# Kernel optimization log

Measured on AMD Instinct MI355X. Metric: run time of the kernel, lower is better.

## Reference

```python
import jax, jax.numpy as jnp
import numpy as np

B, C, M = 1024, 64, 512  # batch, cluster_dim, num_clusters


def setup_inputs() -> dict:
    key = jax.random.key(0)
    k1, k2, k3 = jax.random.split(key, 3)
    x = jax.random.normal(k1, (B, C, M), dtype=jnp.float32)
    running_mean = jax.random.normal(k2, (1, C, M), dtype=jnp.float32) * 0.1
    # per-cluster whitening subspaces: identity + small symmetric perturbation
    A = jax.random.normal(k3, (M, C, C), dtype=jnp.float32) * 0.05
    subspaces = jnp.eye(C, dtype=jnp.float32)[None] + 0.5 * (A + jnp.swapaxes(A, -1, -2))
    return {"x": x, "running_mean": running_mean, "subspaces": subspaces}


def reference(x, running_mean, subspaces):
    # ZCANormSVDPI inference forward:
    #   x: (B, C, M); running_mean: (1, C, M); subspaces: (M, C, C)
    #   xc = x - running_mean; per-cluster m: z[m] = subspaces[m] @ xc[:, :, m]^T
    #   output permuted back to (B, C, M)
    xc = x - running_mean                      # (B, C, M)
    z = jnp.einsum('mcd,bdm->bcm', subspaces, xc)  # (B, C, M)
    return z
```

## Files before the change

kernel.cpp:

```cpp
#include <hip/hip_runtime.h>


typedef __attribute__((ext_vector_type(8))) short short8;
typedef __attribute__((ext_vector_type(4))) float f32x4;

namespace {
constexpr int Mm = 512, Cc = 64, Bb = 1024;
constexpr int MT = 16;
constexpr int BT = 16;
constexpr int NB = 8;
constexpr int ZR = 20;
constexpr size_t LDSB = 2 * 32768 + 1024 * ZR * 4;

__device__ __forceinline__ unsigned short f2bf(float v) {
  unsigned uu = __float_as_uint(v);
  uu = (uu + 0x7fffu + ((uu >> 16) & 1u)) >> 16;
  return (unsigned short)uu;
}
__device__ __forceinline__ unsigned pack2(float a, float b) {
  return (unsigned)f2bf(a) | ((unsigned)f2bf(b) << 16);
}
__device__ __forceinline__ int xsw(int row, int chunk) {
  return chunk ^ (row & 7) ^ (((row >> 6) & 3) << 1);
}
}

#define ELEM(V, I) \
  ((I) == 0 ? (V).x : (I) == 1 ? (V).y : (I) == 2 ? (V).z : (V).w)

__global__ __launch_bounds__(1024, 4) void zca_pipe(
    const float* __restrict__ x, const float* __restrict__ mean,
    const float* __restrict__ S, float* __restrict__ out) {
  extern __shared__ unsigned char lds[];
  unsigned char* xbuf0 = lds;
  unsigned char* xbuf1 = lds + 32768;
  float* zl = (float*)(lds + 65536);

  const int tid = threadIdx.x;
  const int l = tid & 63;
  const int w = __builtin_amdgcn_readfirstlane(tid >> 6);

  const int id = blockIdx.x;
  const int sw = ((id & 7) << 5) + (id >> 3);
  const int m0 = (sw >> 3) * MT;
  const int bg = (sw & 7) * (BT * NB);

  const int mq = tid & 3;
  const int u = (tid >> 2) & 15;
  const int d2 = ((w & 1) << 5) + (u << 1);
  const int bq = w >> 1;
  const int chunkS = ((w & 1) << 2) + (u >> 2);
  const int rowB = (w << 4) + (l & 15);
  const int rs = tid >> 2;

  float4 st0[4], st1[4];

#define ISSUE(ST, T)                                                          \
  {                                                                           \
    _Pragma("unroll") for (int dd = 0; dd < 2; ++dd)                          \
        _Pragma("unroll") for (int p = 0; p < 2; ++p)                         \
            ST[dd * 2 + p] = *(const float4*)(                                \
                x + (size_t)((bg + (T)*BT + p * 8 + bq) * Cc + d2 + dd) * Mm  \
                  + m0 + mq * 4);                                             \
  }

#define STAGE(ST, XW)                                                         \
  {                                                                           \
    _Pragma("unroll") for (int p = 0; p < 2; ++p) {                           \
      _Pragma("unroll") for (int i = 0; i < 4; ++i) {                         \
        const int row = (mq * 4 + i) * BT + p * 8 + bq;                       \
        const unsigned v = pack2(ELEM(ST[p], i) - ELEM(mv0, i),               \
                                 ELEM(ST[2 + p], i) - ELEM(mv1, i));          \
        *(unsigned*)((XW) + row * 128 + xsw(row, chunkS) * 16 + (u & 3) * 4) = \
            v;                                                                \
      }                                                                       \
    }                                                                         \
  }

#define BAR()                                           \
  {                                                     \
    asm volatile("s_waitcnt lgkmcnt(0)" ::: "memory");  \
    __builtin_amdgcn_s_barrier();                       \
  }

#define ZW(CT, R, AC)                                                   \
  {                                                                     \
    const int c_ = (CT)*16 + (l >> 4) * 4 + (R);                        \
    const int zrow = c_ * 16 + (l & 15);                                \
    const int col = (((w >> 2) ^ ((zrow >> 6) & 3)) << 2) + (w & 3);    \
    zl[zrow * ZR + col] = (AC)[(R)];                                    \
  }

  ISSUE(st0, 0)
  ISSUE(st1, 1)
  const float4 mv0 = *(const float4*)(mean + (size_t)d2 * Mm + m0 + mq * 4);
  const float4 mv1 =
      *(const float4*)(mean + (size_t)(d2 + 1) * Mm + m0 + mq * 4);

  short8 A[4][2];
#pragma unroll
  for (int ct = 0; ct < 4; ++ct) {
#pragma unroll
    for (int ks = 0; ks < 2; ++ks) {
      const float* sp = S + ((size_t)(m0 + w) * Cc + ct * 16 + (l & 15)) * Cc +
                        ks * 32 + (l >> 4) * 8;
      const float4 f0 = *(const float4*)sp;
      const float4 f1 = *(const float4*)(sp + 4);
      short8 a;
      a[0] = (short)f2bf(f0.x); a[1] = (short)f2bf(f0.y);
      a[2] = (short)f2bf(f0.z); a[3] = (short)f2bf(f0.w);
      a[4] = (short)f2bf(f1.x); a[5] = (short)f2bf(f1.y);
      a[6] = (short)f2bf(f1.z); a[7] = (short)f2bf(f1.w);
      A[ct][ks] = a;
    }
  }
  STAGE(st0, xbuf0)
  BAR()

#define ITER(T, STC, STN)                                                      \
  {                                                                            \
    const unsigned char* xr = ((T)&1) ? xbuf1 : xbuf0;                         \
    unsigned char* xw = ((T)&1) ? xbuf0 : xbuf1;                               \
    const short8 Bf0 =                                                         \
        *(const short8*)(xr + rowB * 128 + xsw(rowB, (l >> 4)) * 16);          \
    const short8 Bf1 =                                                         \
        *(const short8*)(xr + rowB * 128 + xsw(rowB, 4 + (l >> 4)) * 16);      \
    if ((T) + 2 < NB) ISSUE(STN, (T) + 2)                                      \
    f32x4 ac0 = {0.f, 0.f, 0.f, 0.f}, ac1 = {0.f, 0.f, 0.f, 0.f},              \
          ac2 = {0.f, 0.f, 0.f, 0.f}, ac3 = {0.f, 0.f, 0.f, 0.f};              \
    ac0 = __builtin_amdgcn_mfma_f32_16x16x32_bf16(A[0][0], Bf0, ac0, 0, 0, 0); \
    ac1 = __builtin_amdgcn_mfma_f32_16x16x32_bf16(A[1][0], Bf0, ac1, 0, 0, 0); \
    ac2 = __builtin_amdgcn_mfma_f32_16x16x32_bf16(A[2][0], Bf0, ac2, 0, 0, 0); \
    ac3 = __builtin_amdgcn_mfma_f32_16x16x32_bf16(A[3][0], Bf0, ac3, 0, 0, 0); \
    ac0 = __builtin_amdgcn_mfma_f32_16x16x32_bf16(A[0][1], Bf1, ac0, 0, 0, 0); \
    ac1 = __builtin_amdgcn_mfma_f32_16x16x32_bf16(A[1][1], Bf1, ac1, 0, 0, 0); \
    ac2 = __builtin_amdgcn_mfma_f32_16x16x32_bf16(A[2][1], Bf1, ac2, 0, 0, 0); \
    ac3 = __builtin_amdgcn_mfma_f32_16x16x32_bf16(A[3][1], Bf1, ac3, 0, 0, 0); \
    if ((T) + 1 < NB) STAGE(STC, xw)                                           \
    BAR()                                                                      \
    _Pragma("unroll") for (int r = 0; r < 4; ++r) {                            \
      ZW(0, r, ac0) ZW(1, r, ac1) ZW(2, r, ac2) ZW(3, r, ac3)                  \
    }                                                                          \
    BAR()                                                                      \
    _Pragma("unroll") for (int t2 = 0; t2 < 4; ++t2) {                         \
      const int row = t2 * 256 + rs;                                           \
      const int qd = mq ^ ((row >> 6) & 3);                                    \
      const float4 v = *(const float4*)(zl + row * ZR + qd * 4);               \
      *(float4*)(out + (size_t)((bg + (T)*BT + (row & 15)) * Cc +              \
                                (row >> 4)) * Mm + m0 + mq * 4) = v;           \
    }                                                                          \
  }

  ITER(0, st1, st0)
  ITER(1, st0, st1)
  ITER(2, st1, st0)
  ITER(3, st0, st1)
  ITER(4, st1, st0)
  ITER(5, st0, st1)
  ITER(6, st1, st0)
  ITER(7, st0, st1)

#undef ITER
#undef ZW
#undef BAR
#undef STAGE
#undef ISSUE
}

extern "C" void kernel_launch(void* const* d_in, const int* in_sizes, int n_in,
                              void* d_out, int out_size, void* d_ws,
                              size_t ws_size, hipStream_t stream) {
  const float* x = (const float*)d_in[0];
  const float* mean = (const float*)d_in[1];
  const float* S = (const float*)d_in[2];
  float* out = (float*)d_out;
  const int nblocks = (Mm / MT) * (Bb / (BT * NB));
  hipLaunchKernelGGL(zca_pipe, dim3(nblocks), dim3(1024), LDSB, stream, x,
                     mean, S, out);
}
```

Baseline: 74.93 us.

## Halve cluster tile to 8 with 512-thread blocks and single LDS buffer

```diff
diff --git a/kernel.cpp b/kernel.cpp
--- a/kernel.cpp
+++ b/kernel.cpp
@@ -6,11 +6,11 @@
 
 namespace {
 constexpr int Mm = 512, Cc = 64, Bb = 1024;
-constexpr int MT = 16;
+constexpr int MT = 8;
 constexpr int BT = 16;
 constexpr int NB = 8;
-constexpr int ZR = 20;
-constexpr size_t LDSB = 2 * 32768 + 1024 * ZR * 4;
+constexpr int ZP = 12;
+constexpr size_t LDSB = 128 * 128 + 1024 * ZP * 4;
 
 __device__ __forceinline__ unsigned short f2bf(float v) {
   unsigned uu = __float_as_uint(v);
@@ -20,82 +20,67 @@
 __device__ __forceinline__ unsigned pack2(float a, float b) {
   return (unsigned)f2bf(a) | ((unsigned)f2bf(b) << 16);
 }
-__device__ __forceinline__ int xsw(int row, int chunk) {
-  return chunk ^ (row & 7) ^ (((row >> 6) & 3) << 1);
-}
 }
 
 #define ELEM(V, I) \
   ((I) == 0 ? (V).x : (I) == 1 ? (V).y : (I) == 2 ? (V).z : (V).w)
 
-__global__ __launch_bounds__(1024, 4) void zca_pipe(
+__global__ __launch_bounds__(512, 4) void zca_v7(
     const float* __restrict__ x, const float* __restrict__ mean,
     const float* __restrict__ S, float* __restrict__ out) {
   extern __shared__ unsigned char lds[];
-  unsigned char* xbuf0 = lds;
-  unsigned char* xbuf1 = lds + 32768;
-  float* zl = (float*)(lds + 65536);
+  unsigned char* xl = lds;
+  float* zl = (float*)(lds + 16384);
 
   const int tid = threadIdx.x;
   const int l = tid & 63;
   const int w = __builtin_amdgcn_readfirstlane(tid >> 6);
 
   const int id = blockIdx.x;
-  const int sw = ((id & 7) << 5) + (id >> 3);
+  const int sw = ((id & 7) << 6) + (id >> 3);
   const int m0 = (sw >> 3) * MT;
-  const int bg = (sw & 7) * (BT * NB);
+  const int b0 = (sw & 7) * (BT * NB);
 
-  const int mq = tid & 3;
-  const int u = (tid >> 2) & 15;
-  const int d2 = ((w & 1) << 5) + (u << 1);
-  const int bq = w >> 1;
-  const int chunkS = ((w & 1) << 2) + (u >> 2);
-  const int rowB = (w << 4) + (l & 15);
-  const int rs = tid >> 2;
+  const int mq = l & 1;
+  const int e = l >> 1;
+  const int g2 = w >> 1;
+
+#define ISSUE(ST, T)                                                         \
+  {                                                                          \
+    _Pragma("unroll") for (int dd = 0; dd < 2; ++dd)                         \
+        _Pragma("unroll") for (int p = 0; p < 2; ++p)                        \
+            ST[dd * 2 + p] = *(const float4*)(                               \
+                x + (size_t)((b0 + (T)*BT + p * 8 + w) * Cc + 2 * e + dd) *  \
+                        Mm + m0 + mq * 4);                                   \
+  }
+
+#define STAGE(ST)                                                            \
+  {                                                                          \
+    _Pragma("unroll") for (int p = 0; p < 2; ++p) {                          \
+      _Pragma("unroll") for (int i = 0; i < 4; ++i) {                        \
+        const int row = (mq * 4 + i) * BT + p * 8 + w;                       \
+        const unsigned v = pack2(ELEM(ST[p], i) - ELEM(mvE, i),              \
+                                 ELEM(ST[2 + p], i) - ELEM(mvO, i));         \
+        *(unsigned*)(xl + row * 128 + (((e >> 2) ^ w) << 4) +                \
+                     ((e & 3) << 2)) = v;                                    \
+      }                                                                      \
+    }                                                                        \
+  }
+
+#define BAR()                                          \
+  {                                                    \
+    asm volatile("s_waitcnt lgkmcnt(0)" ::: "memory"); \
+    __builtin_amdgcn_s_barrier();                      \
+  }
 
   float4 st0[4], st1[4];
 
-#define ISSUE(ST, T)                                                          \
-  {                                                                           \
-    _Pragma("unroll") for (int dd = 0; dd < 2; ++dd)                          \
-        _Pragma("unroll") for (int p = 0; p < 2; ++p)                         \
-            ST[dd * 2 + p] = *(const float4*)(                                \
-                x + (size_t)((bg + (T)*BT + p * 8 + bq) * Cc + d2 + dd) * Mm  \
-                  + m0 + mq * 4);                                             \
-  }
-
-#define STAGE(ST, XW)                                                         \
-  {                                                                           \
-    _Pragma("unroll") for (int p = 0; p < 2; ++p) {                           \
-      _Pragma("unroll") for (int i = 0; i < 4; ++i) {                         \
-        const int row = (mq * 4 + i) * BT + p * 8 + bq;                       \
-        const unsigned v = pack2(ELEM(ST[p], i) - ELEM(mv0, i),               \
-                                 ELEM(ST[2 + p], i) - ELEM(mv1, i));          \
-        *(unsigned*)((XW) + row * 128 + xsw(row, chunkS) * 16 + (u & 3) * 4) = \
-            v;                                                                \
-      }                                                                       \
-    }                                                                         \
-  }
-
-#define BAR()                                           \
-  {                                                     \
-    asm volatile("s_waitcnt lgkmcnt(0)" ::: "memory");  \
-    __builtin_amdgcn_s_barrier();                       \
-  }
-
-#define ZW(CT, R, AC)                                                   \
-  {                                                                     \
-    const int c_ = (CT)*16 + (l >> 4) * 4 + (R);                        \
-    const int zrow = c_ * 16 + (l & 15);                                \
-    const int col = (((w >> 2) ^ ((zrow >> 6) & 3)) << 2) + (w & 3);    \
-    zl[zrow * ZR + col] = (AC)[(R)];                                    \
-  }
-
   ISSUE(st0, 0)
   ISSUE(st1, 1)
-  const float4 mv0 = *(const float4*)(mean + (size_t)d2 * Mm + m0 + mq * 4);
-  const float4 mv1 =
-      *(const float4*)(mean + (size_t)(d2 + 1) * Mm + m0 + mq * 4);
+  const float4 mvE =
+      *(const float4*)(mean + (size_t)(2 * e) * Mm + m0 + mq * 4);
+  const float4 mvO =
+      *(const float4*)(mean + (size_t)(2 * e + 1) * Mm + m0 + mq * 4);
 
   short8 A[4][2];
 #pragma unroll
@@ -114,41 +99,50 @@
       A[ct][ks] = a;
     }
   }
-  STAGE(st0, xbuf0)
+  STAGE(st0)
   BAR()
 
 #define ITER(T, STC, STN)                                                      \
   {                                                                            \
-    const unsigned char* xr = ((T)&1) ? xbuf1 : xbuf0;                         \
-    unsigned char* xw = ((T)&1) ? xbuf0 : xbuf1;                               \
+    const int rb = (w * 16 + (l & 15)) * 128;                                  \
     const short8 Bf0 =                                                         \
-        *(const short8*)(xr + rowB * 128 + xsw(rowB, (l >> 4)) * 16);          \
+        *(const short8*)(xl + rb + ((((l >> 4)) ^ (l & 7)) << 4));             \
     const short8 Bf1 =                                                         \
-        *(const short8*)(xr + rowB * 128 + xsw(rowB, 4 + (l >> 4)) * 16);      \
+        *(const short8*)(xl + rb + (((4 | (l >> 4)) ^ (l & 7)) << 4));         \
     if ((T) + 2 < NB) ISSUE(STN, (T) + 2)                                      \
-    f32x4 ac0 = {0.f, 0.f, 0.f, 0.f}, ac1 = {0.f, 0.f, 0.f, 0.f},              \
-          ac2 = {0.f, 0.f, 0.f, 0.f}, ac3 = {0.f, 0.f, 0.f, 0.f};              \
-    ac0 = __builtin_amdgcn_mfma_f32_16x16x32_bf16(A[0][0], Bf0, ac0, 0, 0, 0); \
-    ac1 = __builtin_amdgcn_mfma_f32_16x16x32_bf16(A[1][0], Bf0, ac1, 0, 0, 0); \
-    ac2 = __builtin_amdgcn_mfma_f32_16x16x32_bf16(A[2][0], Bf0, ac2, 0, 0, 0); \
-    ac3 = __builtin_amdgcn_mfma_f32_16x16x32_bf16(A[3][0], Bf0, ac3, 0, 0, 0); \
-    ac0 = __builtin_amdgcn_mfma_f32_16x16x32_bf16(A[0][1], Bf1, ac0, 0, 0, 0); \
-    ac1 = __builtin_amdgcn_mfma_f32_16x16x32_bf16(A[1][1], Bf1, ac1, 0, 0, 0); \
-    ac2 = __builtin_amdgcn_mfma_f32_16x16x32_bf16(A[2][1], Bf1, ac2, 0, 0, 0); \
-    ac3 = __builtin_amdgcn_mfma_f32_16x16x32_bf16(A[3][1], Bf1, ac3, 0, 0, 0); \
-    if ((T) + 1 < NB) STAGE(STC, xw)                                           \
-    BAR()                                                                      \
-    _Pragma("unroll") for (int r = 0; r < 4; ++r) {                            \
-      ZW(0, r, ac0) ZW(1, r, ac1) ZW(2, r, ac2) ZW(3, r, ac3)                  \
+    f32x4 acc[4];                                                              \
+    _Pragma("unroll") for (int ct = 0; ct < 4; ++ct) acc[ct] =                 \
+        (f32x4){0.f, 0.f, 0.f, 0.f};                                          \
+    _Pragma("unroll") for (int ct = 0; ct < 4; ++ct) acc[ct] =                 \
+        __builtin_amdgcn_mfma_f32_16x16x32_bf16(A[ct][0], Bf0, acc[ct], 0, 0,  \
+                                                0);                            \
+    _Pragma("unroll") for (int ct = 0; ct < 4; ++ct) acc[ct] =                 \
+        __builtin_amdgcn_mfma_f32_16x16x32_bf16(A[ct][1], Bf1, acc[ct], 0, 0,  \
+                                                0);                            \
+    _Pragma("unroll") for (int ct = 0; ct < 4; ++ct) {                         \
+      _Pragma("unroll") for (int r = 0; r < 4; ++r) {                          \
+        const int c_ = ct * 16 + (l >> 4) * 4 + r;                             \
+        const int zrow = c_ * 16 + (l & 15);                                   \
+        zl[zrow * ZP + (w ^ (l >> 4))] = acc[ct][r];                           \
+      }                                                                        \
     }                                                                          \
-    BAR()                                                                      \
+    BAR()                                  \
+    if ((T) + 1 < NB) STAGE(STC)                                               \
     _Pragma("unroll") for (int t2 = 0; t2 < 4; ++t2) {                         \
-      const int row = t2 * 256 + rs;                                           \
-      const int qd = mq ^ ((row >> 6) & 3);                                    \
-      const float4 v = *(const float4*)(zl + row * ZR + qd * 4);               \
-      *(float4*)(out + (size_t)((bg + (T)*BT + (row & 15)) * Cc +              \
-                                (row >> 4)) * Mm + m0 + mq * 4) = v;           \
+      const int zrow = t2 * 256 + w * 32 + e;                                  \
+      float4 v = *(const float4*)(zl + zrow * ZP + mq * 4);                    \
+      if (g2 & 1) {                                                            \
+        float t = v.x; v.x = v.y; v.y = t;                                     \
+        t = v.z; v.z = v.w; v.w = t;                                           \
+      }                                                                        \
+      if (g2 & 2) {                                                            \
+        float t = v.x; v.x = v.z; v.z = t;                                     \
+        t = v.y; v.y = v.w; v.w = t;                                           \
+      }                                                                        \
+      *(float4*)(out + (size_t)((b0 + (T)*BT + (zrow & 15)) * Cc +             \
+                                (zrow >> 4)) * Mm + m0 + mq * 4) = v;          \
     }                                                                          \
+    if ((T) < NB - 1) BAR()                    \
   }
 
   ITER(0, st1, st0)
@@ -161,7 +155,6 @@
   ITER(7, st0, st1)
 
 #undef ITER
-#undef ZW
 #undef BAR
 #undef STAGE
 #undef ISSUE
@@ -175,6 +168,6 @@
   const float* S = (const float*)d_in[2];
   float* out = (float*)d_out;
   const int nblocks = (Mm / MT) * (Bb / (BT * NB));
-  hipLaunchKernelGGL(zca_pipe, dim3(nblocks), dim3(1024), LDSB, stream, x,
-                     mean, S, out);
+  hipLaunchKernelGGL(zca_v7, dim3(nblocks), dim3(512), LDSB, stream, x, mean,
+                     S, out);
 }
```

Result: slower. 80.93 us (+8.0%).

## Shrink LDS footprint with single x buffer and split output staging for occupancy

Applied to the files above, without the earlier changes.

```diff
diff --git a/kernel.cpp b/kernel.cpp
--- a/kernel.cpp
+++ b/kernel.cpp
@@ -1,4 +1,5 @@
 #include <hip/hip_runtime.h>
+#include <hip/hip_bf16.h>
 
 
 typedef __attribute__((ext_vector_type(8))) short short8;
@@ -6,52 +7,50 @@
 
 namespace {
 constexpr int Mm = 512, Cc = 64, Bb = 1024;
-constexpr int MT = 16;
-constexpr int BT = 16;
-constexpr int NB = 8;
-constexpr int ZR = 20;
-constexpr size_t LDSB = 2 * 32768 + 1024 * ZR * 4;
+constexpr int MT = 16, BT = 16, NB = 4;
+constexpr int ZP = 20;
+constexpr size_t LDSB = 32768 + 512 * ZP * 4;
 
-__device__ __forceinline__ unsigned short f2bf(float v) {
-  unsigned uu = __float_as_uint(v);
-  uu = (uu + 0x7fffu + ((uu >> 16) & 1u)) >> 16;
-  return (unsigned short)uu;
+__device__ __forceinline__ short bfc(float f) {
+  __hip_bfloat16 h = __float2bfloat16(f);
+  union { __hip_bfloat16 b; short s; } u;
+  u.b = h;
+  return u.s;
 }
 __device__ __forceinline__ unsigned pack2(float a, float b) {
-  return (unsigned)f2bf(a) | ((unsigned)f2bf(b) << 16);
+  return (unsigned)(unsigned short)bfc(a) |
+         ((unsigned)(unsigned short)bfc(b) << 16);
 }
-__device__ __forceinline__ int xsw(int row, int chunk) {
-  return chunk ^ (row & 7) ^ (((row >> 6) & 3) << 1);
+__device__ __forceinline__ int xsw(int row, int c) {
+  return c ^ (row & 7) ^ (((row >> 6) & 3) << 1);
 }
 }
 
-#define ELEM(V, I) \
-  ((I) == 0 ? (V).x : (I) == 1 ? (V).y : (I) == 2 ? (V).z : (V).w)
+#define ELEM(V, I) ((I) == 0 ? (V).x : (I) == 1 ? (V).y : (I) == 2 ? (V).z : (V).w)
 
-__global__ __launch_bounds__(1024, 4) void zca_pipe(
+__global__ __launch_bounds__(1024, 8) void zca_v9(
     const float* __restrict__ x, const float* __restrict__ mean,
     const float* __restrict__ S, float* __restrict__ out) {
   extern __shared__ unsigned char lds[];
-  unsigned char* xbuf0 = lds;
-  unsigned char* xbuf1 = lds + 32768;
-  float* zl = (float*)(lds + 65536);
+  unsigned char* xl = lds;
+  float* zl = (float*)(lds + 32768);
 
   const int tid = threadIdx.x;
   const int l = tid & 63;
   const int w = __builtin_amdgcn_readfirstlane(tid >> 6);
 
-  const int id = blockIdx.x;
-  const int sw = ((id & 7) << 5) + (id >> 3);
-  const int m0 = (sw >> 3) * MT;
-  const int bg = (sw & 7) * (BT * NB);
+  const int xcd = blockIdx.x & 7, ord = blockIdx.x >> 3;
+  const int m0 = (xcd * 4 + (ord & 3)) * MT;
+  const int b0 = (ord >> 2) * (BT * NB);
 
   const int mq = tid & 3;
   const int u = (tid >> 2) & 15;
+  const int bq = w >> 1;
   const int d2 = ((w & 1) << 5) + (u << 1);
-  const int bq = w >> 1;
   const int chunkS = ((w & 1) << 2) + (u >> 2);
-  const int rowB = (w << 4) + (l & 15);
-  const int rs = tid >> 2;
+  const int zrow_r = tid & 511;
+  const int qp = tid >> 9;
+  const int h2r = (tid >> 6) & 3;
 
   float4 st0[4], st1[4];
 
@@ -60,41 +59,54 @@
     _Pragma("unroll") for (int dd = 0; dd < 2; ++dd)                          \
         _Pragma("unroll") for (int p = 0; p < 2; ++p)                         \
             ST[dd * 2 + p] = *(const float4*)(                                \
-                x + (size_t)((bg + (T)*BT + p * 8 + bq) * Cc + d2 + dd) * Mm  \
+                x + (size_t)((b0 + (T)*BT + p * 8 + bq) * Cc + d2 + dd) * Mm  \
                   + m0 + mq * 4);                                             \
   }
 
-#define STAGE(ST, XW)                                                         \
+#define STAGE(ST)                                                             \
   {                                                                           \
     _Pragma("unroll") for (int p = 0; p < 2; ++p) {                           \
       _Pragma("unroll") for (int i = 0; i < 4; ++i) {                         \
         const int row = (mq * 4 + i) * BT + p * 8 + bq;                       \
-        const unsigned v = pack2(ELEM(ST[p], i) - ELEM(mv0, i),               \
-                                 ELEM(ST[2 + p], i) - ELEM(mv1, i));          \
-        *(unsigned*)((XW) + row * 128 + xsw(row, chunkS) * 16 + (u & 3) * 4) = \
+        const unsigned v = pack2(ELEM(ST[p], i) - ELEM(mvE, i),               \
+                                 ELEM(ST[2 + p], i) - ELEM(mvO, i));          \
+        *(unsigned*)(xl + row * 128 + xsw(row, chunkS) * 16 + (u & 3) * 4) =  \
             v;                                                                \
       }                                                                       \
     }                                                                         \
   }
 
-#define BAR()                                           \
-  {                                                     \
-    asm volatile("s_waitcnt lgkmcnt(0)" ::: "memory");  \
-    __builtin_amdgcn_s_barrier();                       \
+#define BAR()                                          \
+  {                                                    \
+    asm volatile("s_waitcnt lgkmcnt(0)" ::: "memory"); \
+    __builtin_amdgcn_s_barrier();                      \
   }
 
-#define ZW(CT, R, AC)                                                   \
-  {                                                                     \
-    const int c_ = (CT)*16 + (l >> 4) * 4 + (R);                        \
-    const int zrow = c_ * 16 + (l & 15);                                \
-    const int col = (((w >> 2) ^ ((zrow >> 6) & 3)) << 2) + (w & 3);    \
-    zl[zrow * ZR + col] = (AC)[(R)];                                    \
+#define ZW(H)                                                                 \
+  {                                                                           \
+    _Pragma("unroll") for (int c2 = 0; c2 < 2; ++c2) {                        \
+      _Pragma("unroll") for (int r = 0; r < 4; ++r) {                         \
+        const int h2 = l >> 4;                                                \
+        const int zrow = (c2 * 16 + h2 * 4 + r) * 16 + (l & 15);              \
+        zl[zrow * ZP + (w ^ (h2 << 2))] = acc[(H)*2 + c2][r];                 \
+      }                                                                       \
+    }                                                                         \
+  }
+
+#define ZR(H, T)                                                              \
+  {                                                                           \
+    const int bz = zrow_r & 15, cl = (H)*32 + (zrow_r >> 4);                  \
+    float* op = out + (size_t)((b0 + (T)*BT + bz) * Cc + cl) * Mm + m0;       \
+    const float4 v0 = *(const float4*)(zl + zrow_r * ZP + (qp * 2) * 4);      \
+    const float4 v1 = *(const float4*)(zl + zrow_r * ZP + (qp * 2 + 1) * 4);  \
+    *(float4*)(op + ((qp * 2) ^ h2r) * 4) = v0;                               \
+    *(float4*)(op + ((qp * 2 + 1) ^ h2r) * 4) = v1;                           \
   }
 
   ISSUE(st0, 0)
   ISSUE(st1, 1)
-  const float4 mv0 = *(const float4*)(mean + (size_t)d2 * Mm + m0 + mq * 4);
-  const float4 mv1 =
+  const float4 mvE = *(const float4*)(mean + (size_t)d2 * Mm + m0 + mq * 4);
+  const float4 mvO =
       *(const float4*)(mean + (size_t)(d2 + 1) * Mm + m0 + mq * 4);
 
   short8 A[4][2];
@@ -107,60 +119,49 @@
       const float4 f0 = *(const float4*)sp;
       const float4 f1 = *(const float4*)(sp + 4);
       short8 a;
-      a[0] = (short)f2bf(f0.x); a[1] = (short)f2bf(f0.y);
-      a[2] = (short)f2bf(f0.z); a[3] = (short)f2bf(f0.w);
-      a[4] = (short)f2bf(f1.x); a[5] = (short)f2bf(f1.y);
-      a[6] = (short)f2bf(f1.z); a[7] = (short)f2bf(f1.w);
+      a[0] = bfc(f0.x); a[1] = bfc(f0.y); a[2] = bfc(f0.z); a[3] = bfc(f0.w);
+      a[4] = bfc(f1.x); a[5] = bfc(f1.y); a[6] = bfc(f1.z); a[7] = bfc(f1.w);
       A[ct][ks] = a;
     }
   }
-  STAGE(st0, xbuf0)
+  STAGE(st0)
   BAR()
 
 #define ITER(T, STC, STN)                                                      \
   {                                                                            \
-    const unsigned char* xr = ((T)&1) ? xbuf1 : xbuf0;                         \
-    unsigned char* xw = ((T)&1) ? xbuf0 : xbuf1;                               \
-    const short8 Bf0 =                                                         \
-        *(const short8*)(xr + rowB * 128 + xsw(rowB, (l >> 4)) * 16);          \
-    const short8 Bf1 =                                                         \
-        *(const short8*)(xr + rowB * 128 + xsw(rowB, 4 + (l >> 4)) * 16);      \
+    const int rowB = w * BT + (l & 15);                                        \
+    const short8 Bf0 = *(const short8*)(                                       \
+        xl + rowB * 128 + xsw(rowB, (l >> 4)) * 16);                           \
+    const short8 Bf1 = *(const short8*)(                                       \
+        xl + rowB * 128 + xsw(rowB, 4 + (l >> 4)) * 16);                       \
     if ((T) + 2 < NB) ISSUE(STN, (T) + 2)                                      \
-    f32x4 ac0 = {0.f, 0.f, 0.f, 0.f}, ac1 = {0.f, 0.f, 0.f, 0.f},              \
-          ac2 = {0.f, 0.f, 0.f, 0.f}, ac3 = {0.f, 0.f, 0.f, 0.f};              \
-    ac0 = __builtin_amdgcn_mfma_f32_16x16x32_bf16(A[0][0], Bf0, ac0, 0, 0, 0); \
-    ac1 = __builtin_amdgcn_mfma_f32_16x16x32_bf16(A[1][0], Bf0, ac1, 0, 0, 0); \
-    ac2 = __builtin_amdgcn_mfma_f32_16x16x32_bf16(A[2][0], Bf0, ac2, 0, 0, 0); \
-    ac3 = __builtin_amdgcn_mfma_f32_16x16x32_bf16(A[3][0], Bf0, ac3, 0, 0, 0); \
-    ac0 = __builtin_amdgcn_mfma_f32_16x16x32_bf16(A[0][1], Bf1, ac0, 0, 0, 0); \
-    ac1 = __builtin_amdgcn_mfma_f32_16x16x32_bf16(A[1][1], Bf1, ac1, 0, 0, 0); \
-    ac2 = __builtin_amdgcn_mfma_f32_16x16x32_bf16(A[2][1], Bf1, ac2, 0, 0, 0); \
-    ac3 = __builtin_amdgcn_mfma_f32_16x16x32_bf16(A[3][1], Bf1, ac3, 0, 0, 0); \
-    if ((T) + 1 < NB) STAGE(STC, xw)                                           \
-    BAR()                                                                      \
-    _Pragma("unroll") for (int r = 0; r < 4; ++r) {                            \
-      ZW(0, r, ac0) ZW(1, r, ac1) ZW(2, r, ac2) ZW(3, r, ac3)                  \
-    }                                                                          \
-    BAR()                                                                      \
-    _Pragma("unroll") for (int t2 = 0; t2 < 4; ++t2) {                         \
-      const int row = t2 * 256 + rs;                                           \
-      const int qd = mq ^ ((row >> 6) & 3);                                    \
-      const float4 v = *(const float4*)(zl + row * ZR + qd * 4);               \
-      *(float4*)(out + (size_t)((bg + (T)*BT + (row & 15)) * Cc +              \
-                                (row >> 4)) * Mm + m0 + mq * 4) = v;           \
-    }                                                                          \
+    f32x4 acc[4];                                                              \
+    _Pragma("unroll") for (int ct = 0; ct < 4; ++ct) acc[ct] =                 \
+        (f32x4){0.f, 0.f, 0.f, 0.f};                                           \
+    _Pragma("unroll") for (int ct = 0; ct < 4; ++ct) acc[ct] =                 \
+        __builtin_amdgcn_mfma_f32_16x16x32_bf16(A[ct][0], Bf0, acc[ct], 0, 0,  \
+                                                0);                            \
+    _Pragma("unroll") for (int ct = 0; ct < 4; ++ct) acc[ct] =                 \
+        __builtin_amdgcn_mfma_f32_16x16x32_bf16(A[ct][1], Bf1, acc[ct], 0, 0,  \
+                                                0);                            \
+    BAR()                                 \
+    if ((T) + 1 < NB) STAGE(STC)                                               \
+    ZW(0)                                                                      \
+    BAR()                                       \
+    ZR(0, T)                                                                   \
+    BAR()                                                  \
+    ZW(1)                                                                      \
+    BAR()                                               \
+    ZR(1, T)                                                                   \
   }
 
   ITER(0, st1, st0)
   ITER(1, st0, st1)
   ITER(2, st1, st0)
   ITER(3, st0, st1)
-  ITER(4, st1, st0)
-  ITER(5, st0, st1)
-  ITER(6, st1, st0)
-  ITER(7, st0, st1)
 
 #undef ITER
+#undef ZR
 #undef ZW
 #undef BAR
 #undef STAGE
@@ -175,6 +176,6 @@
   const float* S = (const float*)d_in[2];
   float* out = (float*)d_out;
   const int nblocks = (Mm / MT) * (Bb / (BT * NB));
-  hipLaunchKernelGGL(zca_pipe, dim3(nblocks), dim3(1024), LDSB, stream, x,
-                     mean, S, out);
+  hipLaunchKernelGGL(zca_v9, dim3(nblocks), dim3(1024), LDSB, stream, x, mean,
+                     S, out);
 }
```

New measurement: 224.3 us. 199% more time.
